# Optimization experiments

Measured on AMD Instinct MI355X. Metric: run time of the kernel, lower is better.

The kernel has to match this reference:

```python
import jax, jax.numpy as jnp
import numpy as np

N, T, D = 64, 2048, 256


def setup_inputs() -> dict:
    key = jax.random.key(0)
    k1, k2, k3, k4 = jax.random.split(key, 4)
    query = jax.random.normal(k1, (N, D), dtype=jnp.float32)
    key_t = jax.random.normal(k2, (N, T, D), dtype=jnp.float32)
    value = jax.random.normal(k3, (N, T, D), dtype=jnp.float32)
    lens = jax.random.randint(k4, (N,), 1, T + 1, dtype=jnp.int64)  # valid lengths in [1, T]
    return {"query": query, "key": key_t, "value": value, "lens": lens}


def reference(query, key, value, lens):
    # energy[n, t] = <key[n, t, :], query[n, :]>
    energy = jnp.einsum("ntd,nd->nt", key, query)
    attention = jax.nn.softmax(energy, axis=1)  # [N, T]
    # mask out positions >= lens[n], then renormalize over valid positions
    attention_mask = (jnp.arange(T)[None, :] < lens[:, None]).astype(attention.dtype)
    mask_attention = attention * attention_mask
    norm_attention = mask_attention / jnp.sum(mask_attention, axis=1, keepdims=True)
    # context[n, d] = sum_t norm_attention[n, t] * value[n, t, d]
    context = jnp.einsum("nt,ntd->nd", norm_attention, value)
    return (context, norm_attention)
```

## Files before the change

### kernel.cpp

```cpp
#include <hip/hip_runtime.h>


#define N_B 64
#define T_S 2048
#define D_S 256
#define TPB 256
#define RC 64
#define NC (T_S / RC)

__global__ __launch_bounds__(TPB) void fused_kernel(
    const float* __restrict__ q, const float* __restrict__ k,
    const float* __restrict__ v, const int* __restrict__ lens,
    float* __restrict__ p_out, float2* __restrict__ mzc,
    float* __restrict__ Oc) {
  const int n = blockIdx.y;
  const int c = blockIdx.x;
  const int L = lens[n];
  const int t0 = c * RC;
  if (t0 >= L) return;
  const int tend = min(t0 + RC, L);
  const int tid = threadIdx.x;
  const int lane = tid & 63;
  const int wave = tid >> 6;

  __shared__ float e_sh[RC];
  __shared__ float p_sh[RC];
  __shared__ float4 part[TPB];

  if (tid < RC) e_sh[tid] = -1e30f;
  __syncthreads();

  const float4 qv = reinterpret_cast<const float4*>(q + (size_t)n * D_S)[lane];
  const float* kbase = k + (size_t)n * T_S * D_S;
  int t = t0 + wave;
  for (; t + 4 < tend; t += 8) {
    const float4 a =
        reinterpret_cast<const float4*>(kbase + (size_t)t * D_S)[lane];
    const float4 b =
        reinterpret_cast<const float4*>(kbase + (size_t)(t + 4) * D_S)[lane];
    float s0 = a.x * qv.x + a.y * qv.y + a.z * qv.z + a.w * qv.w;
    float s1 = b.x * qv.x + b.y * qv.y + b.z * qv.z + b.w * qv.w;
#pragma unroll
    for (int off = 32; off > 0; off >>= 1) {
      s0 += __shfl_xor(s0, off, 64);
      s1 += __shfl_xor(s1, off, 64);
    }
    if (lane == 0) {
      e_sh[t - t0] = s0;
      e_sh[t + 4 - t0] = s1;
    }
  }
  if (t < tend) {
    const float4 a =
        reinterpret_cast<const float4*>(kbase + (size_t)t * D_S)[lane];
    float s0 = a.x * qv.x + a.y * qv.y + a.z * qv.z + a.w * qv.w;
#pragma unroll
    for (int off = 32; off > 0; off >>= 1) s0 += __shfl_xor(s0, off, 64);
    if (lane == 0) e_sh[t - t0] = s0;
  }
  __syncthreads();

  if (wave == 0) {
    const float e = e_sh[lane];
    float m = e;
#pragma unroll
    for (int off = 32; off > 0; off >>= 1) m = fmaxf(m, __shfl_xor(m, off, 64));
    const float pv = __expf(e - m);
    float z = pv;
#pragma unroll
    for (int off = 32; off > 0; off >>= 1) z += __shfl_xor(z, off, 64);
    p_sh[lane] = pv;
    p_out[(size_t)n * T_S + t0 + lane] = pv;
    if (lane == 0) mzc[n * NC + c] = make_float2(m, z);
  }
  __syncthreads();

  const int dg = tid & 63;
  const int tg = tid >> 6;
  const int nv = tend - t0;
  const float* vbase = v + (size_t)n * T_S * D_S + (size_t)t0 * D_S;

  float4 acc0 = {0.f, 0.f, 0.f, 0.f}, acc1 = {0.f, 0.f, 0.f, 0.f};
  int j = tg;
  for (; j + 4 < nv; j += 8) {
    const float4 v0 =
        reinterpret_cast<const float4*>(vbase + (size_t)j * D_S)[dg];
    const float4 v1 =
        reinterpret_cast<const float4*>(vbase + (size_t)(j + 4) * D_S)[dg];
    const float a0 = p_sh[j], a1 = p_sh[j + 4];
    acc0.x = fmaf(a0, v0.x, acc0.x);
    acc0.y = fmaf(a0, v0.y, acc0.y);
    acc0.z = fmaf(a0, v0.z, acc0.z);
    acc0.w = fmaf(a0, v0.w, acc0.w);
    acc1.x = fmaf(a1, v1.x, acc1.x);
    acc1.y = fmaf(a1, v1.y, acc1.y);
    acc1.z = fmaf(a1, v1.z, acc1.z);
    acc1.w = fmaf(a1, v1.w, acc1.w);
  }
  if (j < nv) {
    const float4 v0 =
        reinterpret_cast<const float4*>(vbase + (size_t)j * D_S)[dg];
    const float a0 = p_sh[j];
    acc0.x = fmaf(a0, v0.x, acc0.x);
    acc0.y = fmaf(a0, v0.y, acc0.y);
    acc0.z = fmaf(a0, v0.z, acc0.z);
    acc0.w = fmaf(a0, v0.w, acc0.w);
  }
  acc0.x += acc1.x;
  acc0.y += acc1.y;
  acc0.z += acc1.z;
  acc0.w += acc1.w;

  part[tid] = acc0;
  __syncthreads();
  if (tg == 0) {
    float4 r = part[dg];
    const float4 r1 = part[dg + 64], r2 = part[dg + 128], r3 = part[dg + 192];
    r.x += r1.x + r2.x + r3.x;
    r.y += r1.y + r2.y + r3.y;
    r.z += r1.z + r2.z + r3.z;
    r.w += r1.w + r2.w + r3.w;
    reinterpret_cast<float4*>(Oc + ((size_t)(n * NC + c)) * D_S)[dg] = r;
  }
}

__global__ __launch_bounds__(TPB) void merge_kernel(
    const int* __restrict__ lens, const float* __restrict__ p_in,
    const float2* __restrict__ mzc, const float* __restrict__ Oc,
    float* __restrict__ out_ctx, float* __restrict__ out_attn) {
  const int n = blockIdx.x;
  const int L = lens[n];
  const int nc = (L + RC - 1) / RC;
  const int tid = threadIdx.x;
  __shared__ float s_sh[NC];

  if (tid < 64) {
    float m = -1e30f, z = 0.f;
    if (tid < nc) {
      const float2 mz = mzc[n * NC + tid];
      m = mz.x;
      z = mz.y;
    }
    float M = m;
#pragma unroll
    for (int off = 32; off > 0; off >>= 1) M = fmaxf(M, __shfl_xor(M, off, 64));
    const float sc = __expf(m - M);
    float zs = z * sc;
#pragma unroll
    for (int off = 32; off > 0; off >>= 1) zs += __shfl_xor(zs, off, 64);
    if (tid < NC) s_sh[tid] = sc / zs;
  }
  __syncthreads();

#pragma unroll
  for (int i = 0; i < T_S / TPB; ++i) {
    const int t = i * TPB + tid;
    const float a = (t < L) ? p_in[(size_t)n * T_S + t] * s_sh[t >> 6] : 0.f;
    out_attn[(size_t)n * T_S + t] = a;
  }

  float acc = 0.f;
  const float* ob = Oc + (size_t)n * NC * D_S + tid;
#pragma unroll
  for (int c2 = 0; c2 < NC; ++c2) acc = fmaf(s_sh[c2], ob[c2 * D_S], acc);
  out_ctx[(size_t)n * D_S + tid] = acc;
}

extern "C" void kernel_launch(void* const* d_in, const int* in_sizes, int n_in,
                              void* d_out, int out_size, void* d_ws,
                              size_t ws_size, hipStream_t stream) {
  const float* query = (const float*)d_in[0];
  const float* key = (const float*)d_in[1];
  const float* value = (const float*)d_in[2];
  const int* lens = (const int*)d_in[3];

  float* out_ctx = (float*)d_out;
  float* out_attn = (float*)d_out + N_B * D_S;

  float* p = (float*)d_ws;
  float2* mzc = (float2*)(p + (size_t)N_B * T_S);
  float* Oc = (float*)(mzc + N_B * NC);

  const dim3 grid(NC, N_B);
  fused_kernel<<<grid, TPB, 0, stream>>>(query, key, value, lens, p, mzc, Oc);
  merge_kernel<<<N_B, TPB, 0, stream>>>(lens, p, mzc, Oc, out_ctx, out_attn);
}
```

Measured before the change: 260.2 us.

## Raise memory-level parallelism in K/V streaming and split merge across blocks

The K dot-product phase now has each 16-lane group own one row. Each wave runs four fixed unrolled row groups with nontemporal float4 loads, and q is staged once in shared memory. The V accumulation is fully unrolled with four independent accumulators and no tail bounds checks. Rows past the valid length are still loaded but get zero weight from p_sh. The merge kernel is split into 4 blocks per batch row, each handling a slice of attention and context, to raise parallelism in the second launch. The intent is more loads in flight on a bandwidth-bound stream. The cost is extra reads for partial chunks and more register use.

```diff
diff --git a/kernel.cpp b/kernel.cpp
--- a/kernel.cpp
+++ b/kernel.cpp
@@ -8,55 +8,64 @@
 #define RC 64
 #define NC (T_S / RC)
 
+typedef __attribute__((ext_vector_type(4))) float f4;
+typedef __attribute__((ext_vector_type(2))) float f2;
+
+__device__ __forceinline__ f4 ntload4(const float* p) {
+  return __builtin_nontemporal_load((const f4*)p);
+}
+__device__ __forceinline__ f4 fma4(float s, f4 a, f4 b) {
+  b.x = fmaf(s, a.x, b.x);
+  b.y = fmaf(s, a.y, b.y);
+  b.z = fmaf(s, a.z, b.z);
+  b.w = fmaf(s, a.w, b.w);
+  return b;
+}
+
 __global__ __launch_bounds__(TPB) void fused_kernel(
     const float* __restrict__ q, const float* __restrict__ k,
     const float* __restrict__ v, const int* __restrict__ lens,
     float* __restrict__ p_out, float2* __restrict__ mzc,
     float* __restrict__ Oc) {
-  const int n = blockIdx.y;
-  const int c = blockIdx.x;
+  const int n = blockIdx.y, c = blockIdx.x;
   const int L = lens[n];
   const int t0 = c * RC;
   if (t0 >= L) return;
   const int tend = min(t0 + RC, L);
   const int tid = threadIdx.x;
-  const int lane = tid & 63;
-  const int wave = tid >> 6;
+  const int lane = tid & 63, wave = tid >> 6;
 
+  __shared__ f4 q_sh[64];
   __shared__ float e_sh[RC];
   __shared__ float p_sh[RC];
-  __shared__ float4 part[TPB];
+  __shared__ f4 part[TPB];
 
+  if (tid < 64) q_sh[tid] = ((const f4*)(q + (size_t)n * D_S))[tid];
   if (tid < RC) e_sh[tid] = -1e30f;
   __syncthreads();
 
-  const float4 qv = reinterpret_cast<const float4*>(q + (size_t)n * D_S)[lane];
-  const float* kbase = k + (size_t)n * T_S * D_S;
-  int t = t0 + wave;
-  for (; t + 4 < tend; t += 8) {
-    const float4 a =
-        reinterpret_cast<const float4*>(kbase + (size_t)t * D_S)[lane];
-    const float4 b =
-        reinterpret_cast<const float4*>(kbase + (size_t)(t + 4) * D_S)[lane];
-    float s0 = a.x * qv.x + a.y * qv.y + a.z * qv.z + a.w * qv.w;
-    float s1 = b.x * qv.x + b.y * qv.y + b.z * qv.z + b.w * qv.w;
+  {
+    const int s = lane & 15, qd = lane >> 4;
+    const float* kb = k + (size_t)n * T_S * D_S + s * 4;
+    const int rbase = t0 + wave * 16 + qd;
 #pragma unroll
-    for (int off = 32; off > 0; off >>= 1) {
-      s0 += __shfl_xor(s0, off, 64);
-      s1 += __shfl_xor(s1, off, 64);
+    for (int g = 0; g < 4; ++g) {
+      const int r = rbase + g * 4;
+      const float* krow = kb + (size_t)r * D_S;
+      float acc = 0.f;
+#pragma unroll
+      for (int i = 0; i < 4; ++i) {
+        const f4 kv = ntload4(krow + i * 64);
+        const f4 qv = q_sh[i * 16 + s];
+        acc = fmaf(kv.x, qv.x, acc);
+        acc = fmaf(kv.y, qv.y, acc);
+        acc = fmaf(kv.z, qv.z, acc);
+        acc = fmaf(kv.w, qv.w, acc);
+      }
+#pragma unroll
+      for (int off = 8; off > 0; off >>= 1) acc += __shfl_xor(acc, off, 64);
+      if (s == 0 && r < tend) e_sh[r - t0] = acc;
     }
-    if (lane == 0) {
-      e_sh[t - t0] = s0;
-      e_sh[t + 4 - t0] = s1;
-    }
-  }
-  if (t < tend) {
-    const float4 a =
-        reinterpret_cast<const float4*>(kbase + (size_t)t * D_S)[lane];
-    float s0 = a.x * qv.x + a.y * qv.y + a.z * qv.z + a.w * qv.w;
-#pragma unroll
-    for (int off = 32; off > 0; off >>= 1) s0 += __shfl_xor(s0, off, 64);
-    if (lane == 0) e_sh[t - t0] = s0;
   }
   __syncthreads();
 
@@ -75,52 +84,26 @@
   }
   __syncthreads();
 
-  const int dg = tid & 63;
-  const int tg = tid >> 6;
-  const int nv = tend - t0;
-  const float* vbase = v + (size_t)n * T_S * D_S + (size_t)t0 * D_S;
-
-  float4 acc0 = {0.f, 0.f, 0.f, 0.f}, acc1 = {0.f, 0.f, 0.f, 0.f};
-  int j = tg;
-  for (; j + 4 < nv; j += 8) {
-    const float4 v0 =
-        reinterpret_cast<const float4*>(vbase + (size_t)j * D_S)[dg];
-    const float4 v1 =
-        reinterpret_cast<const float4*>(vbase + (size_t)(j + 4) * D_S)[dg];
-    const float a0 = p_sh[j], a1 = p_sh[j + 4];
-    acc0.x = fmaf(a0, v0.x, acc0.x);
-    acc0.y = fmaf(a0, v0.y, acc0.y);
-    acc0.z = fmaf(a0, v0.z, acc0.z);
-    acc0.w = fmaf(a0, v0.w, acc0.w);
-    acc1.x = fmaf(a1, v1.x, acc1.x);
-    acc1.y = fmaf(a1, v1.y, acc1.y);
-    acc1.z = fmaf(a1, v1.z, acc1.z);
-    acc1.w = fmaf(a1, v1.w, acc1.w);
+  const int dg = tid & 63, tg = tid >> 6;
+  const float* vb = v + (size_t)n * T_S * D_S + (size_t)t0 * D_S + dg * 4;
+  f4 a0 = {0.f, 0.f, 0.f, 0.f}, a1 = a0, a2 = a0, a3 = a0;
+#pragma unroll
+  for (int j = 0; j < 4; ++j) {
+    const int r0 = j * 16 + tg;
+    const f4 v0 = ntload4(vb + (size_t)r0 * D_S);
+    const f4 v1 = ntload4(vb + (size_t)(r0 + 4) * D_S);
+    const f4 v2 = ntload4(vb + (size_t)(r0 + 8) * D_S);
+    const f4 v3 = ntload4(vb + (size_t)(r0 + 12) * D_S);
+    a0 = fma4(p_sh[r0], v0, a0);
+    a1 = fma4(p_sh[r0 + 4], v1, a1);
+    a2 = fma4(p_sh[r0 + 8], v2, a2);
+    a3 = fma4(p_sh[r0 + 12], v3, a3);
   }
-  if (j < nv) {
-    const float4 v0 =
-        reinterpret_cast<const float4*>(vbase + (size_t)j * D_S)[dg];
-    const float a0 = p_sh[j];
-    acc0.x = fmaf(a0, v0.x, acc0.x);
-    acc0.y = fmaf(a0, v0.y, acc0.y);
-    acc0.z = fmaf(a0, v0.z, acc0.z);
-    acc0.w = fmaf(a0, v0.w, acc0.w);
-  }
-  acc0.x += acc1.x;
-  acc0.y += acc1.y;
-  acc0.z += acc1.z;
-  acc0.w += acc1.w;
-
-  part[tid] = acc0;
+  part[tid] = (a0 + a1) + (a2 + a3);
   __syncthreads();
   if (tg == 0) {
-    float4 r = part[dg];
-    const float4 r1 = part[dg + 64], r2 = part[dg + 128], r3 = part[dg + 192];
-    r.x += r1.x + r2.x + r3.x;
-    r.y += r1.y + r2.y + r3.y;
-    r.z += r1.z + r2.z + r3.z;
-    r.w += r1.w + r2.w + r3.w;
-    reinterpret_cast<float4*>(Oc + ((size_t)(n * NC + c)) * D_S)[dg] = r;
+    const f4 r = part[dg] + part[dg + 64] + part[dg + 128] + part[dg + 192];
+    ((f4*)(Oc + ((size_t)(n * NC + c)) * D_S))[dg] = r;
   }
 }
 
@@ -128,11 +111,12 @@
     const int* __restrict__ lens, const float* __restrict__ p_in,
     const float2* __restrict__ mzc, const float* __restrict__ Oc,
     float* __restrict__ out_ctx, float* __restrict__ out_attn) {
-  const int n = blockIdx.x;
+  const int n = blockIdx.y, cx = blockIdx.x;
   const int L = lens[n];
   const int nc = (L + RC - 1) / RC;
   const int tid = threadIdx.x;
   __shared__ float s_sh[NC];
+  __shared__ float cpart[TPB];
 
   if (tid < 64) {
     float m = -1e30f, z = 0.f;
@@ -152,18 +136,32 @@
   }
   __syncthreads();
 
-#pragma unroll
-  for (int i = 0; i < T_S / TPB; ++i) {
-    const int t = i * TPB + tid;
-    const float a = (t < L) ? p_in[(size_t)n * T_S + t] * s_sh[t >> 6] : 0.f;
-    out_attn[(size_t)n * T_S + t] = a;
+  {
+    const int t = cx * (T_S / 4) + tid * 2;
+    const f2 p = *(const f2*)(p_in + (size_t)n * T_S + t);
+    const float sc = s_sh[t >> 6];
+    f2 a;
+    a.x = (t < L) ? p.x * sc : 0.f;
+    a.y = (t + 1 < L) ? p.y * sc : 0.f;
+    *(f2*)(out_attn + (size_t)n * T_S + t) = a;
   }
 
-  float acc = 0.f;
-  const float* ob = Oc + (size_t)n * NC * D_S + tid;
+  {
+    const int d = cx * 64 + (tid & 63);
+    const int cg = tid >> 6;
+    const float* ob = Oc + (size_t)n * NC * D_S + d;
+    float acc = 0.f;
 #pragma unroll
-  for (int c2 = 0; c2 < NC; ++c2) acc = fmaf(s_sh[c2], ob[c2 * D_S], acc);
-  out_ctx[(size_t)n * D_S + tid] = acc;
+    for (int kk = 0; kk < 8; ++kk) {
+      const int cc = cg + kk * 4;
+      acc = fmaf(s_sh[cc], ob[(size_t)cc * D_S], acc);
+    }
+    cpart[tid] = acc;
+    __syncthreads();
+    if (tid < 64)
+      out_ctx[(size_t)n * D_S + d] =
+          (cpart[tid] + cpart[tid + 64]) + (cpart[tid + 128] + cpart[tid + 192]);
+  }
 }
 
 extern "C" void kernel_launch(void* const* d_in, const int* in_sizes, int n_in,
@@ -181,7 +179,8 @@
   float2* mzc = (float2*)(p + (size_t)N_B * T_S);
   float* Oc = (float*)(mzc + N_B * NC);
 
-  const dim3 grid(NC, N_B);
-  fused_kernel<<<grid, TPB, 0, stream>>>(query, key, value, lens, p, mzc, Oc);
-  merge_kernel<<<N_B, TPB, 0, stream>>>(lens, p, mzc, Oc, out_ctx, out_attn);
+  const dim3 grid1(NC, N_B);
+  fused_kernel<<<grid1, TPB, 0, stream>>>(query, key, value, lens, p, mzc, Oc);
+  const dim3 grid2(4, N_B);
+  merge_kernel<<<grid2, TPB, 0, stream>>>(lens, p, mzc, Oc, out_ctx, out_attn);
 }
```

Result: faster. 241.8 us (-7.1%).
